# Optimization experiments

Measured on AMD Instinct MI355X. Metric: run time of the kernel, lower is better.

Reference implementation:

```python
import jax, jax.numpy as jnp
import numpy as np

NX, NH, NY, T = 128, 512, 1, 16384


def setup_inputs() -> dict:
    key = jax.random.key(0)
    ks = jax.random.split(key, 10)
    s = 0.01
    return {
        "x_t": jax.random.normal(ks[0], (T, 1), dtype=jnp.float32),
        "Wf": jax.random.normal(ks[1], (NH, NX), dtype=jnp.float32) * s,
        "Uf": jax.random.normal(ks[2], (NH, NH), dtype=jnp.float32) * s,
        "bf": jnp.zeros((NH,), dtype=jnp.float32),
        "Wi": jax.random.normal(ks[3], (NH, NX), dtype=jnp.float32) * s,
        "Ui": jax.random.normal(ks[4], (NH, NH), dtype=jnp.float32) * s,
        "bi": jnp.zeros((NH,), dtype=jnp.float32),
        "Wo": jax.random.normal(ks[5], (NH, NX), dtype=jnp.float32) * s,
        "Uo": jax.random.normal(ks[6], (NH, NH), dtype=jnp.float32) * s,
        "bo": jnp.zeros((NH,), dtype=jnp.float32),
        "Wc": jax.random.normal(ks[7], (NH, NX), dtype=jnp.float32) * s,
        "Uc": jax.random.normal(ks[8], (NH, NH), dtype=jnp.float32) * s,
        "bc": jnp.zeros((NH,), dtype=jnp.float32),
        "Ahy": jax.random.normal(ks[9], (NY, NH), dtype=jnp.float32) * s,
        "by": jnp.zeros((NY,), dtype=jnp.float32),
    }


def reference(x_t, Wf, Uf, bf, Wi, Ui, bi, Wo, Uo, bo, Wc, Uc, bc, Ahy, by):
    # x_t: (T, 1) univariate series; sliding windows of length Nx feed each step.
    Tlen = x_t.shape[0]
    Nx = Wf.shape[1]
    Nh = Wf.shape[0]
    steps = Tlen - Nx  # number of recurrent steps

    x = x_t[:, 0]  # (T,)
    idx = jnp.arange(steps)[:, None] + jnp.arange(Nx)[None, :]
    Xw = x[idx]  # (steps, Nx) sliding windows

    # Precompute input projections for all steps (batched GEMMs).
    xf = Xw @ Wf.T + bf  # (steps, Nh)
    xi = Xw @ Wi.T + bi
    xo = Xw @ Wo.T + bo
    xc = Xw @ Wc.T + bc

    def step(carry, inp):
        h, c = carry
        xf_t, xi_t, xo_t, xc_t = inp
        f = jax.nn.sigmoid(xf_t + Uf @ h)
        i = jax.nn.sigmoid(xi_t + Ui @ h)
        o = jax.nn.sigmoid(xo_t + Uo @ h)
        g = jnp.tanh(xc_t + Uc @ h)
        c = f * c + i * g
        h = o * jnp.tanh(c)
        mu = Ahy @ h + by  # (Ny,)
        return (h, c), mu

    init = (jnp.zeros((Nh,), x_t.dtype), jnp.zeros((Nh,), x_t.dtype))
    _, mu = jax.lax.scan(step, init, (xf, xi, xo, xc))
    return mu  # (steps, Ny) == (T-Nx, 1), matching torch's stack(...).unsqueeze(1)
```

## Files before the change

### kernel.cpp

```cpp
#include <hip/hip_runtime.h>

#define NHID 512
#define NXW  128
#define TLEN 16384
#define STEPS (TLEN - NXW)
#define G    32
#define B    512
#define RPW  16
#define RSLOTS 8

#define FOR4(M)  M(0) M(1) M(2) M(3)
#define FOR16(M) M(0) M(1) M(2) M(3) M(4) M(5) M(6) M(7) \
                 M(8) M(9) M(10) M(11) M(12) M(13) M(14) M(15)

__device__ __forceinline__ float sigmoid_f(float v) { return 1.f / (1.f + __expf(-v)); }
__device__ __forceinline__ float tanh_f(float v)    { return 1.f - 2.f / (1.f + __expf(2.f * v)); }

#define AL(p) __hip_atomic_load((p), __ATOMIC_RELAXED, __HIP_MEMORY_SCOPE_AGENT)

__device__ __forceinline__ void stagger_delay(float& v) {
    #pragma unroll
    for (int i = 0; i < 75; ++i)
        asm volatile("v_fmac_f32 %0, %1, %1" : "+v"(v) : "v"(1.0000001f));
}

__launch_bounds__(B, 2)
__global__ void lstm_persistent(
    const float* x,
    const float* Wf, const float* Uf, const float* bf,
    const float* Wi, const float* Ui, const float* bi,
    const float* Wo, const float* Uo, const float* bo,
    const float* Wc, const float* Uc, const float* bc,
    unsigned long long* ring,
    float* h_hist)
{
    __shared__ float x_win[256];
    __shared__ __align__(16) float h_buf[8][64];
    __shared__ float partials[2][B];

    const int tid = threadIdx.x;
    const int g   = blockIdx.x;
    const int w   = tid >> 6;
    const int l   = tid & 63;
    const int q   = l >> 4;
    const int row = g * RPW + (l & 15);

    const float* Utab[4] = {Uf, Ui, Uo, Uc};
    const float* Wtab[4] = {Wf, Wi, Wo, Wc};
    const float* Btab[4] = {bf, bi, bo, bc};

    const float4* Up = (const float4*)(Utab[q] + (size_t)row * NHID + w * 64);
    #define DECLU(i) float4 u##i = Up[i];
    FOR16(DECLU)
    const float4* Wp = (const float4*)(Wtab[q] + row * NXW + w * 16);
    #define DECLW(i) float4 wv##i = Wp[i];
    FOR4(DECLW)
    #define PIN(r) asm volatile("" : "+v"(r.x), "+v"(r.y), "+v"(r.z), "+v"(r.w));
    #define PINU(i) PIN(u##i)
    FOR16(PINU)
    #define PINW(i) PIN(wv##i)
    FOR4(PINW)

    float bias = 0.f, c_prev = 0.f;
    if (w == 0) bias = Btab[q][row];

    h_buf[w][l] = 0.f;

    for (int t = 0; t < STEPS; ++t) {
        if ((t & 127) == 0) {
            __syncthreads();
            if (tid < 256) {
                int gi = t + tid;
                x_win[tid] = (gi < TLEN) ? x[gi] : 0.f;
            }
            __syncthreads();
        }

        const unsigned want = (unsigned)(t - 1);
        const unsigned long long* src =
            ring + ((size_t)((t - 1) & (RSLOTS - 1)) << 9) + (w * 64 + l);
        unsigned long long vv = 0;
        if (t > 0) vv = AL(src);

        float xa0 = 0.f, xa1 = 0.f;
        {
            const int xb = (t & 127) + w * 16;
            #define XF(i, A) A += wv##i.x * x_win[xb + 4*i]     \
                                + wv##i.y * x_win[xb + 4*i + 1] \
                                + wv##i.z * x_win[xb + 4*i + 2] \
                                + wv##i.w * x_win[xb + 4*i + 3];
            XF(0, xa0) XF(1, xa1) XF(2, xa0) XF(3, xa1)
        }
        const float xacc = xa0 + xa1;

        if (t > 0) {
            if ((unsigned)(vv >> 32) != want) {
                unsigned long long b1 = AL(src);
                float dly = xacc;
                stagger_delay(dly);
                asm volatile("" :: "v"(dly));
                unsigned long long b2 = AL(src);
                int guard = 1 << 20;
                for (;;) {
                    if ((unsigned)(vv >> 32) == want) break;
                    vv = AL(src);
                    if ((unsigned)(b1 >> 32) == want) { vv = b1; break; }
                    b1 = AL(src);
                    if ((unsigned)(b2 >> 32) == want) { vv = b2; break; }
                    b2 = AL(src);
                    if (--guard == 0) break;
                }
            }
            h_buf[w][l] = __uint_as_float((unsigned)vv);
        }

        float ac0 = xacc, ac1 = 0.f, ac2 = 0.f, ac3 = 0.f;
        const float4* hb4 = (const float4*)h_buf[w];
        #define UF(i, A) { float4 hv = hb4[i];                    \
                           A += u##i.x * hv.x + u##i.y * hv.y     \
                              + u##i.z * hv.z + u##i.w * hv.w; }
        UF(0,  ac0) UF(1,  ac1) UF(2,  ac2) UF(3,  ac3)
        UF(4,  ac0) UF(5,  ac1) UF(6,  ac2) UF(7,  ac3)
        UF(8,  ac0) UF(9,  ac1) UF(10, ac2) UF(11, ac3)
        UF(12, ac0) UF(13, ac1) UF(14, ac2) UF(15, ac3)
        const float acc = (ac0 + ac1) + (ac2 + ac3);

        partials[t & 1][tid] = acc;
        __syncthreads();

        if (w == 0) {
            const float* p = partials[t & 1];
            float r0 = p[64  + l] + p[128 + l];
            float r1 = p[192 + l] + p[256 + l];
            float r2 = p[320 + l] + p[384 + l];
            float r3 = p[448 + l];
            float pre = ((acc + bias) + r0) + ((r1 + r2) + r3);
            float a = (l < 48) ? sigmoid_f(pre) : tanh_f(pre);
            float ai = __shfl(a, l + 16, 64);
            float ao = __shfl(a, l + 32, 64);
            float ag = __shfl(a, l + 48, 64);
            if (l < 16) {
                float c = a * c_prev + ai * ag;
                c_prev = c;
                float h = ao * tanh_f(c);
                unsigned long long pv =
                    ((unsigned long long)(unsigned)t << 32)
                    | (unsigned long long)__float_as_uint(h);
                __hip_atomic_store(
                    ring + ((size_t)(t & (RSLOTS - 1)) << 9) + row, pv,
                    __ATOMIC_RELAXED, __HIP_MEMORY_SCOPE_AGENT);
                h_hist[(size_t)t * NHID + row] = h;
            }
        }
    }
}

__global__ void mu_kernel(const float* __restrict__ h_hist,
                          const float* __restrict__ Ahy,
                          const float* __restrict__ by,
                          float* __restrict__ outp, int steps)
{
    int wave = threadIdx.x >> 6;
    int lane = threadIdx.x & 63;
    int t = blockIdx.x * 4 + wave;
    if (t >= steps) return;
    const float* h = h_hist + (size_t)t * NHID;
    float p = 0.f;
    #pragma unroll
    for (int e = 0; e < 8; e++)
        p += Ahy[e * 64 + lane] * h[e * 64 + lane];
    #pragma unroll
    for (int off = 32; off; off >>= 1) p += __shfl_down(p, off, 64);
    if (lane == 0) outp[t] = p + by[0];
}

extern "C" void kernel_launch(void* const* d_in, const int* in_sizes, int n_in,
                              void* d_out, int out_size, void* d_ws, size_t ws_size,
                              hipStream_t stream)
{
    const float* x  = (const float*)d_in[0];
    const float* Wf = (const float*)d_in[1];
    const float* Uf = (const float*)d_in[2];
    const float* bf = (const float*)d_in[3];
    const float* Wi = (const float*)d_in[4];
    const float* Ui = (const float*)d_in[5];
    const float* bi = (const float*)d_in[6];
    const float* Wo = (const float*)d_in[7];
    const float* Uo = (const float*)d_in[8];
    const float* bo = (const float*)d_in[9];
    const float* Wc = (const float*)d_in[10];
    const float* Uc = (const float*)d_in[11];
    const float* bc = (const float*)d_in[12];
    const float* Ahy = (const float*)d_in[13];
    const float* by  = (const float*)d_in[14];

    unsigned long long* ring = (unsigned long long*)d_ws;
    float* h_hist = (float*)((char*)d_ws + RSLOTS * NHID * 8);

    lstm_persistent<<<G, B, 0, stream>>>(x, Wf, Uf, bf, Wi, Ui, bi,
                                         Wo, Uo, bo, Wc, Uc, bc, ring, h_hist);
    int muBlocks = (STEPS + 3) / 4;
    mu_kernel<<<muBlocks, 256, 0, stream>>>(h_hist, Ahy, by, (float*)d_out, STEPS);
}
```

Before: 26.02 ms.

## Distribute gate reduction and cell update across all waves instead of wave zero

The per-step cross-wave reduction of gate pre-activations is now spread over all eight waves. Each wave reduces two hidden rows using padded shared-memory partials and xor shuffles, then computes the cell update and publishes its h values to the ring. Previously wave 0 alone summed eight partials per lane and did all the gate math. The staggered polling loop with its artificial delay is also replaced by a simple spin loop. This shortens the serial tail of each recurrent step, but every wave now produces ring stores, and dropping the stagger may raise contention on the polled ring lines.

```diff
diff --git a/kernel.cpp b/kernel.cpp
--- a/kernel.cpp
+++ b/kernel.cpp
@@ -8,6 +8,7 @@
 #define B    512
 #define RPW  16
 #define RSLOTS 8
+#define PSTRIDE 65
 
 #define FOR4(M)  M(0) M(1) M(2) M(3)
 #define FOR16(M) M(0) M(1) M(2) M(3) M(4) M(5) M(6) M(7) \
@@ -17,12 +18,7 @@
 __device__ __forceinline__ float tanh_f(float v)    { return 1.f - 2.f / (1.f + __expf(2.f * v)); }
 
 #define AL(p) __hip_atomic_load((p), __ATOMIC_RELAXED, __HIP_MEMORY_SCOPE_AGENT)
-
-__device__ __forceinline__ void stagger_delay(float& v) {
-    #pragma unroll
-    for (int i = 0; i < 75; ++i)
-        asm volatile("v_fmac_f32 %0, %1, %1" : "+v"(v) : "v"(1.0000001f));
-}
+#define ASTR(p, v) __hip_atomic_store((p), (v), __ATOMIC_RELAXED, __HIP_MEMORY_SCOPE_AGENT)
 
 __launch_bounds__(B, 2)
 __global__ void lstm_persistent(
@@ -36,23 +32,30 @@
 {
     __shared__ float x_win[256];
     __shared__ __align__(16) float h_buf[8][64];
-    __shared__ float partials[2][B];
+    __shared__ float partials[2][8 * PSTRIDE];
 
     const int tid = threadIdx.x;
     const int g   = blockIdx.x;
     const int w   = tid >> 6;
     const int l   = tid & 63;
-    const int q   = l >> 4;
-    const int row = g * RPW + (l & 15);
+
+    const int q    = l >> 4;
+    const int rowM = g * RPW + (l & 15);
+
+    const int s    = l & 7;
+    const int oi   = l >> 3;
+    const int tq   = oi >> 1;
+    const int rh   = oi & 1;
+    const int rowT = g * RPW + 2 * w + rh;
 
     const float* Utab[4] = {Uf, Ui, Uo, Uc};
     const float* Wtab[4] = {Wf, Wi, Wo, Wc};
     const float* Btab[4] = {bf, bi, bo, bc};
 
-    const float4* Up = (const float4*)(Utab[q] + (size_t)row * NHID + w * 64);
+    const float4* Up = (const float4*)(Utab[q] + (size_t)rowM * NHID + w * 64);
     #define DECLU(i) float4 u##i = Up[i];
     FOR16(DECLU)
-    const float4* Wp = (const float4*)(Wtab[q] + row * NXW + w * 16);
+    const float4* Wp = (const float4*)(Wtab[q] + rowM * NXW + w * 16);
     #define DECLW(i) float4 wv##i = Wp[i];
     FOR4(DECLW)
     #define PIN(r) asm volatile("" : "+v"(r.x), "+v"(r.y), "+v"(r.z), "+v"(r.w));
@@ -61,8 +64,8 @@
     #define PINW(i) PIN(wv##i)
     FOR4(PINW)
 
-    float bias = 0.f, c_prev = 0.f;
-    if (w == 0) bias = Btab[q][row];
+    const float bias = Btab[tq][rowT];
+    float c_prev = 0.f;
 
     h_buf[w][l] = 0.f;
 
@@ -94,23 +97,9 @@
         const float xacc = xa0 + xa1;
 
         if (t > 0) {
-            if ((unsigned)(vv >> 32) != want) {
-                unsigned long long b1 = AL(src);
-                float dly = xacc;
-                stagger_delay(dly);
-                asm volatile("" :: "v"(dly));
-                unsigned long long b2 = AL(src);
-                int guard = 1 << 20;
-                for (;;) {
-                    if ((unsigned)(vv >> 32) == want) break;
-                    vv = AL(src);
-                    if ((unsigned)(b1 >> 32) == want) { vv = b1; break; }
-                    b1 = AL(src);
-                    if ((unsigned)(b2 >> 32) == want) { vv = b2; break; }
-                    b2 = AL(src);
-                    if (--guard == 0) break;
-                }
-            }
+            int guard = 1 << 20;
+            while ((unsigned)(vv >> 32) != want && --guard)
+                vv = AL(src);
             h_buf[w][l] = __uint_as_float((unsigned)vv);
         }
 
@@ -125,31 +114,31 @@
         UF(12, ac0) UF(13, ac1) UF(14, ac2) UF(15, ac3)
         const float acc = (ac0 + ac1) + (ac2 + ac3);
 
-        partials[t & 1][tid] = acc;
+        partials[t & 1][w * PSTRIDE + l] = acc;
         __syncthreads();
 
-        if (w == 0) {
+        {
             const float* p = partials[t & 1];
-            float r0 = p[64  + l] + p[128 + l];
-            float r1 = p[192 + l] + p[256 + l];
-            float r2 = p[320 + l] + p[384 + l];
-            float r3 = p[448 + l];
-            float pre = ((acc + bias) + r0) + ((r1 + r2) + r3);
-            float a = (l < 48) ? sigmoid_f(pre) : tanh_f(pre);
-            float ai = __shfl(a, l + 16, 64);
-            float ao = __shfl(a, l + 32, 64);
-            float ag = __shfl(a, l + 48, 64);
-            if (l < 16) {
-                float c = a * c_prev + ai * ag;
-                c_prev = c;
-                float h = ao * tanh_f(c);
+            float pre = p[s * PSTRIDE + tq * 16 + 2 * w + rh];
+            pre += __shfl_xor(pre, 1, 64);
+            pre += __shfl_xor(pre, 2, 64);
+            pre += __shfl_xor(pre, 4, 64);
+            pre += bias;
+            const float a = (tq < 3) ? sigmoid_f(pre) : tanh_f(pre);
+            const int bl = l & 15;
+            const float af = __shfl(a, bl,      64);
+            const float ai = __shfl(a, bl + 16, 64);
+            const float ao = __shfl(a, bl + 32, 64);
+            const float ag = __shfl(a, bl + 48, 64);
+            const float c  = af * c_prev + ai * ag;
+            c_prev = c;
+            const float h = ao * tanh_f(c);
+            if (tq == 0 && s == 0) {
                 unsigned long long pv =
                     ((unsigned long long)(unsigned)t << 32)
                     | (unsigned long long)__float_as_uint(h);
-                __hip_atomic_store(
-                    ring + ((size_t)(t & (RSLOTS - 1)) << 9) + row, pv,
-                    __ATOMIC_RELAXED, __HIP_MEMORY_SCOPE_AGENT);
-                h_hist[(size_t)t * NHID + row] = h;
+                ASTR(ring + ((size_t)(t & (RSLOTS - 1)) << 9) + rowT, pv);
+                h_hist[(size_t)t * NHID + rowT] = h;
             }
         }
     }
```

Result: slower. 36.73 ms (+41.1%).
